# Kernel tuning notes

Hardware: AMD Instinct MI355X
Metric: run time of the kernel (lower is better)

Reference implementation:

```python
import jax, jax.numpy as jnp
import numpy as np

EPS = 1e-6  # torch.nn.CosineSimilarity eps


def _emb_sum(table, ids):
    # ids: (N, L) int -> (N, D): gather rows then sum over tokens (EmbeddingBag-sum)
    return table[ids].sum(axis=1)


def _cos_rows(q, M):
    # cosine similarity of vector q (D,) against each row of M (N, D), torch eps semantics:
    # dot / max(||a||*||b||, eps)
    num = M @ q
    den = jnp.maximum(jnp.linalg.norm(M, axis=1) * jnp.linalg.norm(q), EPS)
    return num / den


def setup_inputs() -> dict:
    key = jax.random.key(0)
    ks = jax.random.split(key, 10)
    V, D = 50000, 128
    N_MEM, N_CAND, N_PERS, L, LQ = 65536, 10000, 20, 20, 32
    return {
        "xs": jax.random.randint(ks[0], (1, LQ), 0, V, dtype=jnp.int32),
        "candidates": jax.random.randint(ks[1], (N_CAND, L), 0, V, dtype=jnp.int32),
        "persona": jax.random.randint(ks[2], (N_PERS, L), 0, V, dtype=jnp.int32),
        "keys": jax.random.randint(ks[3], (N_MEM, L), 0, V, dtype=jnp.int32),
        "values": jax.random.randint(ks[4], (N_MEM, L), 0, V, dtype=jnp.int32),
        "label": jax.random.randint(ks[5], (1, LQ), 0, V, dtype=jnp.int32),
        "shared_emb": jax.random.normal(ks[6], (V, D), dtype=jnp.float32),
        "cand_emb": jax.random.normal(ks[7], (V, D), dtype=jnp.float32),
        "R_W": jax.random.normal(ks[8], (D, D), dtype=jnp.float32) * (1.0 / np.sqrt(D)),
        "R2_W": jax.random.normal(ks[9], (D, D), dtype=jnp.float32) * (1.0 / np.sqrt(D)),
    }


def reference(xs, candidates, persona, keys, values, label, shared_emb, cand_emb, R_W, R2_W):
    enc_keys = _emb_sum(shared_emb, keys)        # (N_mem, D)
    enc_values = _emb_sum(shared_emb, values)    # (N_mem, D)
    enc_cands = _emb_sum(cand_emb, candidates)   # (N_cand, D)
    enc_pers = _emb_sum(shared_emb, persona)     # (N_pers, D)

    q = shared_emb[xs].sum(axis=1).reshape(-1)   # (D,)

    for W in (R_W, R2_W):  # loop is hardcoded to 2 hops in the source
        att = jax.nn.softmax(_cos_rows(q, enc_pers))          # (N_pers,)
        hop = (att[:, None] * enc_pers).sum(axis=0)           # (D,)
        q_plus = (q + hop) @ W.T                               # Linear no bias
        att = jax.nn.softmax(_cos_rows(q_plus, enc_keys))     # (N_mem,)
        hop = (att[:, None] * enc_values).sum(axis=0)         # (D,)
        q = (q_plus + hop) @ W.T

    preds = _cos_rows(q, enc_cands)  # (N_cand,)
    return preds
```

## Files before the change

### kernel.cpp

```cpp
#include <hip/hip_runtime.h>
#include <math.h>
#include <stdint.h>

#define D 128
#define EPS 1e-6f
typedef unsigned short u16;


__device__ __forceinline__ float wave_sum(float v) {
#pragma unroll
    for (int off = 32; off > 0; off >>= 1) v += __shfl_xor(v, off, 64);
    return v;
}
__device__ __forceinline__ float halfwave_sum(float v) {
#pragma unroll
    for (int off = 16; off > 0; off >>= 1) v += __shfl_xor(v, off, 32);
    return v;
}

__device__ __forceinline__ float bf2f(u16 h) {
    union { unsigned u; float f; } x;
    x.u = ((unsigned)h) << 16;
    return x.f;
}
__device__ __forceinline__ float bflo(unsigned u) { return bf2f((u16)(u & 0xffff)); }
__device__ __forceinline__ float bfhi(unsigned u) { return bf2f((u16)(u >> 16)); }
__device__ __forceinline__ u16 f2bf(float f) {
    union { float f; unsigned u; } x;
    x.f = f;
    unsigned u = x.u;
    return (u16)((u + 0x7fff + ((u >> 16) & 1)) >> 16);
}
__device__ __forceinline__ unsigned pack2(float a, float b) {
    return (unsigned)f2bf(a) | ((unsigned)f2bf(b) << 16);
}

__global__ void prep_k(const float* __restrict__ semb, u16* __restrict__ tbl,
                       int V, const int* __restrict__ pers, int NP,
                       const int* __restrict__ xs, int LQ,
                       float* __restrict__ enc_pers, float* __restrict__ pnorms,
                       float* __restrict__ st, int nbA) {
    const int tid = threadIdx.x;
    const int bid = blockIdx.x;
    if (bid < nbA) {
        const int n = V * 64;
        const int stride = nbA * 256;
        for (int i = bid * 256 + tid; i < n; i += stride) {
            const int v = i >> 6;
            const int c2 = i & 63;
            const float2 ab = *(const float2*)(semb + (long)v * D + 2 * c2);
            *(unsigned*)(tbl + (long)v * D + 2 * c2) = pack2(ab.x, ab.y);
        }
    } else {
        const int lane = tid & 63;
        const int half = lane >> 5;
        const int hl = lane & 31;
        const int w0 = (bid - nbA) * 4 + (tid >> 6);
        const int npr = NP + 1;
        const int npairs = (npr + 1) >> 1;
        for (int w = w0; w < npairs; w += 12) {
            const int row = 2 * w + half;
            const bool valid = row < npr;
            const int rowc = valid ? row : NP;
            const bool isq = (rowc == NP);
            const int* ids = isq ? xs : (pers + (long)rowc * 20);
            const int L = isq ? LQ : 20;
            int myid = 0;
            if (hl < L) myid = ids[hl];
            float4 acc = {0.f, 0.f, 0.f, 0.f};
            for (int t = 0; t < L; ++t) {
                const int idx = __shfl(myid, (half << 5) + t, 64);
                const float4 e = *(const float4*)(semb + (long)idx * D + 4 * hl);
                acc.x += e.x; acc.y += e.y; acc.z += e.z; acc.w += e.w;
            }
            if (valid) {
                float* outp = isq ? st : (enc_pers + (long)rowc * D);
                *(float4*)(outp + 4 * hl) = acc;
                float sq = acc.x * acc.x + acc.y * acc.y + acc.z * acc.z + acc.w * acc.w;
                sq = halfwave_sum(sq);
                if (hl == 0) {
                    if (isq) st[384] = sqrtf(sq);
                    else pnorms[rowc] = sqrtf(sq);
                }
            }
        }
    }
}

__device__ void persona_dev(const float* __restrict__ pers_rows,
                            const float* __restrict__ pnorms,
                            const float* __restrict__ W, float* __restrict__ st,
                            int NP, float* smem, int tid) {
    float* qsh = smem;
    float* qh = smem + 128;
    float* att = smem + 256;
    float* red = smem + 320;
    if (tid < D) qsh[tid] = st[tid];
    __syncthreads();
    if (tid < NP) {
        float dot = 0.f;
        const float* pr = pers_rows + (long)tid * D;
        for (int d2 = 0; d2 < D; ++d2) dot += pr[d2] * qsh[d2];
        att[tid] = dot / fmaxf(pnorms[tid] * st[384], EPS);
    }
    __syncthreads();
    if (tid == 0) {
        float m = -1e30f;
        for (int p = 0; p < NP; ++p) m = fmaxf(m, att[p]);
        float s = 0.f;
        for (int p = 0; p < NP; ++p) { att[p] = __expf(att[p] - m); s += att[p]; }
        float inv = 1.f / s;
        for (int p = 0; p < NP; ++p) att[p] *= inv;
    }
    __syncthreads();
    if (tid < D) {
        float h = 0.f;
        for (int p = 0; p < NP; ++p) h += att[p] * pers_rows[(long)p * D + tid];
        qh[tid] = qsh[tid] + h;
    }
    __syncthreads();
    float qp = 0.f;
    if (tid < D) {
        for (int d2 = 0; d2 < D; ++d2) qp += W[(long)tid * D + d2] * qh[d2];
        st[128 + tid] = qp;
    }
    float sq = wave_sum(qp * qp);
    if ((tid & 63) == 0 && tid < 128) red[tid >> 6] = sq;
    __syncthreads();
    if (tid == 0) st[385] = sqrtf(red[0] + red[1]);
    if (tid < D) st[256 + tid] = 0.f;
    if (tid < D) st[512 + tid] = 0.f;
    if (tid == 0) { st[386] = 0.f; st[640] = 0.f; }
}

__device__ void mid_dev_s(const float* __restrict__ W1, const float* __restrict__ W2,
                          const float* __restrict__ pers_rows,
                          const float* __restrict__ pnorms,
                          const float* __restrict__ st,
                          float* __restrict__ qp_out, float* __restrict__ qpn_out,
                          float* smem, int tid, int NP) {
    float* qh = smem;
    float* qsh = smem + 128;
    float* att = smem + 256;
    float* red = smem + 320;
    const float inv = 1.f / st[386];
    if (tid < D) qh[tid] = st[128 + tid] + st[256 + tid] * inv;
    __syncthreads();
    float qn = 0.f;
    if (tid < D) {
        for (int d2 = 0; d2 < D; ++d2) qn += W1[(long)tid * D + d2] * qh[d2];
        qsh[tid] = qn;
    }
    float sq = wave_sum(qn * qn);
    if ((tid & 63) == 0 && tid < 128) red[tid >> 6] = sq;
    __syncthreads();
    const float qnorm = sqrtf(red[0] + red[1]);
    if (tid < NP) {
        float dot = 0.f;
        for (int d2 = 0; d2 < D; ++d2) dot += pers_rows[(long)tid * D + d2] * qsh[d2];
        att[tid] = dot / fmaxf(pnorms[tid] * qnorm, EPS);
    }
    __syncthreads();
    if (tid == 0) {
        float m = -1e30f;
        for (int p = 0; p < NP; ++p) m = fmaxf(m, att[p]);
        float s = 0.f;
        for (int p = 0; p < NP; ++p) { att[p] = __expf(att[p] - m); s += att[p]; }
        float is = 1.f / s;
        for (int p = 0; p < NP; ++p) att[p] *= is;
    }
    __syncthreads();
    if (tid < D) {
        float h = 0.f;
        for (int p = 0; p < NP; ++p) h += att[p] * pers_rows[(long)p * D + tid];
        qh[tid] = qsh[tid] + h;
    }
    __syncthreads();
    float qp = 0.f;
    if (tid < D) {
        for (int d2 = 0; d2 < D; ++d2) qp += W2[(long)tid * D + d2] * qh[d2];
        qp_out[tid] = qp;
    }
    float sq2 = wave_sum(qp * qp);
    if ((tid & 63) == 0 && tid < 128) red[tid >> 6] = sq2;
    __syncthreads();
    if (tid == 0) *qpn_out = sqrtf(red[0] + red[1]);
    __syncthreads();
}

__global__ void kvp_k(const u16* __restrict__ tbl, const int* __restrict__ kids,
                      const int* __restrict__ vids, int N,
                      float* __restrict__ kb, u16* __restrict__ vb,
                      float* __restrict__ knorms,
                      const float* __restrict__ enc_pers,
                      const float* __restrict__ pnorms,
                      const float* __restrict__ RW, float* __restrict__ st,
                      int NP) {
    __shared__ float smem[336];
    const int tid = threadIdx.x;
    const int bid = blockIdx.x;
    if (bid == 0) {
        persona_dev(enc_pers, pnorms, RW, st, NP, smem, tid);
        return;
    }
    const int lane = tid & 63;
    const int half = lane >> 5;
    const int hl = lane & 31;
    const int ghw = ((bid - 1) * 256 + tid) >> 5;
    const int nhw = ((gridDim.x - 1) * 256) >> 5;
    for (int i = ghw; i < N; i += nhw) {
        int kid = 0, vid = 0;
        if (hl < 20) {
            kid = kids[(long)i * 20 + hl];
            vid = vids[(long)i * 20 + hl];
        }
        float k0 = 0.f, k1 = 0.f, k2 = 0.f, k3 = 0.f;
        float v0 = 0.f, v1 = 0.f, v2 = 0.f, v3 = 0.f;
#pragma unroll
        for (int t = 0; t < 20; ++t) {
            const int kj = __shfl(kid, (half << 5) + t, 64);
            const int vj = __shfl(vid, (half << 5) + t, 64);
            const ushort4 ke = *(const ushort4*)(tbl + (long)kj * D + 4 * hl);
            const ushort4 ve = *(const ushort4*)(tbl + (long)vj * D + 4 * hl);
            k0 += bf2f(ke.x); k1 += bf2f(ke.y); k2 += bf2f(ke.z); k3 += bf2f(ke.w);
            v0 += bf2f(ve.x); v1 += bf2f(ve.y); v2 += bf2f(ve.z); v3 += bf2f(ve.w);
        }
        float4 kr;
        kr.x = k0; kr.y = k1; kr.z = k2; kr.w = k3;
        *(float4*)(kb + (long)i * D + 4 * hl) = kr;
        uint2 pv;
        pv.x = pack2(v0, v1);
        pv.y = pack2(v2, v3);
        *(uint2*)(vb + (long)i * D + 4 * hl) = pv;
        float sq = halfwave_sum(k0 * k0 + k1 * k1 + k2 * k2 + k3 * k3);
        if (hl == 0) knorms[i] = sqrtf(sq);
    }
}

__global__ void attcv2_k(const float* __restrict__ kb, const u16* __restrict__ vb,
                         const float* __restrict__ knorms,
                         const float* __restrict__ W1, const float* __restrict__ W2,
                         const float* __restrict__ enc_pers,
                         const float* __restrict__ pnorms,
                         float* __restrict__ st, int N, int NP, int hop) {
    __shared__ float msm[324];
    __shared__ float qp_s[128];
    __shared__ float qpn_s;
    __shared__ float rsm[129];
    const int tid = threadIdx.x;
    if (hop == 0) {
        if (tid < 128) qp_s[tid] = st[128 + tid];
        if (tid == 0) qpn_s = st[385];
    } else {
        mid_dev_s(W1, W2, enc_pers, pnorms, st, qp_s, &qpn_s, msm, tid, NP);
    }
    __syncthreads();
    const int lane = tid & 63;
    const int half = lane >> 5;
    const int hl = lane & 31;
    const float4 qp4 = *(const float4*)(qp_s + 4 * hl);
    const float qpn = qpn_s;
    const int aoff = hop ? 512 : 256;
    const int eoff = hop ? 640 : 386;
    const int ghw = (int)((blockIdx.x * blockDim.x + tid) >> 5);
    const int nhw = (int)((gridDim.x * blockDim.x) >> 5);
    float a0 = 0.f, a1 = 0.f, a2 = 0.f, a3 = 0.f;
    float esum = 0.f;
    for (int i = ghw; i < N; i += nhw) {
        const float4 kr = *(const float4*)(kb + (long)i * D + 4 * hl);
        const float part = kr.x * qp4.x + kr.y * qp4.y + kr.z * qp4.z + kr.w * qp4.w;
        const float dot = halfwave_sum(part);
        const float c = dot / fmaxf(knorms[i] * qpn, EPS);
        const float e = __expf(c);
        const uint2 vh = *(const uint2*)(vb + (long)i * D + 4 * hl);
        a0 += e * bflo(vh.x);
        a1 += e * bfhi(vh.x);
        a2 += e * bflo(vh.y);
        a3 += e * bfhi(vh.y);
        if (hl == 0) esum += e;
    }
    a0 += __shfl_xor(a0, 32, 64);
    a1 += __shfl_xor(a1, 32, 64);
    a2 += __shfl_xor(a2, 32, 64);
    a3 += __shfl_xor(a3, 32, 64);
    esum += __shfl_xor(esum, 32, 64);
    if (tid < 129) rsm[tid] = 0.f;
    __syncthreads();
    if (half == 0) {
        atomicAdd(&rsm[4 * hl + 0], a0);
        atomicAdd(&rsm[4 * hl + 1], a1);
        atomicAdd(&rsm[4 * hl + 2], a2);
        atomicAdd(&rsm[4 * hl + 3], a3);
        if (hl == 0) atomicAdd(&rsm[128], esum);
    }
    __syncthreads();
    if (tid < 128) atomicAdd(&st[aoff + tid], rsm[tid]);
    if (tid == 128) atomicAdd(&st[eoff], rsm[128]);
}

__global__ void k5f(const float* __restrict__ W1, const float* __restrict__ W2,
                    const float* __restrict__ enc_pers,
                    const float* __restrict__ pnorms,
                    const float* __restrict__ cemb,
                    const int* __restrict__ cands, int NC, int NP,
                    const float* __restrict__ st, float* __restrict__ out) {
    __shared__ float msm[324];
    __shared__ float qp2_s[128];
    __shared__ float qpn2_s;
    __shared__ float qhf[128];
    __shared__ float qv[D];
    __shared__ float red2[2];
    __shared__ float qns;
    const int tid = threadIdx.x;
    mid_dev_s(W1, W2, enc_pers, pnorms, st, qp2_s, &qpn2_s, msm, tid, NP);
    const float inv2 = 1.f / st[640];
    if (tid < D) qhf[tid] = qp2_s[tid] + st[512 + tid] * inv2;
    __syncthreads();
    float qn = 0.f;
    if (tid < D) {
        for (int d2 = 0; d2 < D; ++d2) qn += W2[(long)tid * D + d2] * qhf[d2];
        qv[tid] = qn;
    }
    float sq = wave_sum(qn * qn);
    if ((tid & 63) == 0 && tid < 128) red2[tid >> 6] = sq;
    __syncthreads();
    if (tid == 0) qns = sqrtf(red2[0] + red2[1]);
    __syncthreads();
    const int lane = tid & 63;
    const int half = lane >> 5;
    const int hl = lane & 31;
    const int gw = (int)((blockIdx.x * blockDim.x + tid) >> 6);
    const int nw = (int)((gridDim.x * blockDim.x) >> 6);
    const float4 q4 = *(const float4*)(qv + 4 * hl);
    const float qnf = qns;
    const int npair = (NC + 1) >> 1;
    for (int p = gw; p < npair; p += nw) {
        const int row = 2 * p + half;
        const bool valid = row < NC;
        const int rowc = valid ? row : (NC - 1);
        int myid = 0;
        if (hl < 20) myid = cands[(long)rowc * 20 + hl];
        float4 acc = {0.f, 0.f, 0.f, 0.f};
#pragma unroll
        for (int t = 0; t < 20; ++t) {
            const int idx = __shfl(myid, (half << 5) + t, 64);
            const float4 e = *(const float4*)(cemb + (long)idx * D + 4 * hl);
            acc.x += e.x; acc.y += e.y; acc.z += e.z; acc.w += e.w;
        }
        float dot = halfwave_sum(acc.x * q4.x + acc.y * q4.y +
                                 acc.z * q4.z + acc.w * q4.w);
        float nsq = halfwave_sum(acc.x * acc.x + acc.y * acc.y +
                                 acc.z * acc.z + acc.w * acc.w);
        if (valid && hl == 0) out[row] = dot / fmaxf(sqrtf(nsq) * qnf, EPS);
    }
}

__global__ void encode_small_p(const float* __restrict__ emb,
                               const int* __restrict__ pers, int NP, int LP,
                               const int* __restrict__ xs, int LQ,
                               float* __restrict__ pers_rows,
                               float* __restrict__ pnorms,
                               float* __restrict__ st) {
    const int lane = threadIdx.x & 63;
    const int half = lane >> 5;
    const int hl = lane & 31;
    int gw = (int)((blockIdx.x * blockDim.x + threadIdx.x) >> 6);
    int nw = (int)((gridDim.x * blockDim.x) >> 6);
    const int npr = NP + 1;
    const int npairs = (npr + 1) >> 1;
    for (int p = gw; p < npairs; p += nw) {
        const int row = 2 * p + half;
        const bool valid = row < npr;
        const int rowc = valid ? row : NP;
        const bool isq = (rowc == NP);
        const int* ids = isq ? xs : (pers + (long)rowc * LP);
        const int L = isq ? LQ : LP;
        int myid = 0;
        if (hl < L) myid = ids[hl];
        float4 acc = {0.f, 0.f, 0.f, 0.f};
        for (int t = 0; t < L; ++t) {
            const int idx = __shfl(myid, (half << 5) + t, 64);
            const float4 e = *(const float4*)(emb + (long)idx * D + 4 * hl);
            acc.x += e.x; acc.y += e.y; acc.z += e.z; acc.w += e.w;
        }
        if (valid) {
            float* outp = isq ? st : (pers_rows + (long)rowc * D);
            *(float4*)(outp + 4 * hl) = acc;
            float sq = acc.x * acc.x + acc.y * acc.y + acc.z * acc.z + acc.w * acc.w;
            sq = halfwave_sum(sq);
            if (hl == 0) {
                if (isq) st[384] = sqrtf(sq);
                else pnorms[rowc] = sqrtf(sq);
            }
        }
    }
}

__global__ void persona_hop(const float* __restrict__ pers_rows,
                            const float* __restrict__ pnorms,
                            const float* __restrict__ W,
                            float* __restrict__ st, int NP) {
    __shared__ float smem[336];
    persona_dev(pers_rows, pnorms, W, st, NP, smem, (int)threadIdx.x);
}

__global__ void mid_hop(const float* __restrict__ W1, const float* __restrict__ W2,
                        const float* __restrict__ pers_rows,
                        const float* __restrict__ pnorms,
                        float* __restrict__ st, int NP) {
    __shared__ float qh[D];
    __shared__ float qsh[D];
    __shared__ float att[64];
    __shared__ float red[2];
    int tid = threadIdx.x;
    float inv = 1.f / st[386];
    qh[tid] = st[128 + tid] + st[256 + tid] * inv;
    __syncthreads();
    float qn = 0.f;
    for (int d2 = 0; d2 < D; ++d2) qn += W1[tid * D + d2] * qh[d2];
    qsh[tid] = qn;
    st[tid] = qn;
    float sq = wave_sum(qn * qn);
    if ((tid & 63) == 0) red[tid >> 6] = sq;
    __syncthreads();
    float qnorm = sqrtf(red[0] + red[1]);
    if (tid == 0) st[384] = qnorm;
    if (tid < NP) {
        float dot = 0.f;
        for (int d2 = 0; d2 < D; ++d2) dot += pers_rows[tid * D + d2] * qsh[d2];
        att[tid] = dot / fmaxf(pnorms[tid] * qnorm, EPS);
    }
    __syncthreads();
    if (tid == 0) {
        float m = -1e30f;
        for (int p = 0; p < NP; ++p) m = fmaxf(m, att[p]);
        float s = 0.f;
        for (int p = 0; p < NP; ++p) { att[p] = __expf(att[p] - m); s += att[p]; }
        float is = 1.f / s;
        for (int p = 0; p < NP; ++p) att[p] *= is;
    }
    __syncthreads();
    float h = 0.f;
    for (int p = 0; p < NP; ++p) h += att[p] * pers_rows[p * D + tid];
    qh[tid] = qsh[tid] + h;
    __syncthreads();
    float qp = 0.f;
    for (int d2 = 0; d2 < D; ++d2) qp += W2[tid * D + d2] * qh[d2];
    st[128 + tid] = qp;
    float sq2 = wave_sum(qp * qp);
    if ((tid & 63) == 0) red[tid >> 6] = sq2;
    __syncthreads();
    if (tid == 0) st[385] = sqrtf(red[0] + red[1]);
    st[256 + tid] = 0.f;
    if (tid == 0) st[386] = 0.f;
}

__global__ void finish_hop(const float* __restrict__ W, float* __restrict__ st) {
    __shared__ float qh[D];
    __shared__ float red[2];
    int tid = threadIdx.x;
    float inv = 1.f / st[386];
    qh[tid] = st[128 + tid] + st[256 + tid] * inv;
    __syncthreads();
    float qn = 0.f;
    for (int d2 = 0; d2 < D; ++d2) qn += W[tid * D + d2] * qh[d2];
    st[tid] = qn;
    float sq = wave_sum(qn * qn);
    if ((tid & 63) == 0) red[tid >> 6] = sq;
    __syncthreads();
    if (tid == 0) st[384] = sqrtf(red[0] + red[1]);
}

__global__ void k5_final(const float* __restrict__ cemb,
                         const int* __restrict__ cands, int NC,
                         const float* __restrict__ st, float* __restrict__ out) {
    const int lane = threadIdx.x & 63;
    const int half = lane >> 5;
    const int hl = lane & 31;
    const int gw = (int)((blockIdx.x * blockDim.x + threadIdx.x) >> 6);
    const int nw = (int)((gridDim.x * blockDim.x) >> 6);
    const float4 q4 = *(const float4*)(st + 4 * hl);
    const float qn = st[384];
    const int npair = (NC + 1) >> 1;
    for (int p = gw; p < npair; p += nw) {
        const int row = 2 * p + half;
        const bool valid = row < NC;
        const int rowc = valid ? row : (NC - 1);
        int myid = 0;
        if (hl < 20) myid = cands[(long)rowc * 20 + hl];
        float4 acc = {0.f, 0.f, 0.f, 0.f};
#pragma unroll
        for (int t = 0; t < 20; ++t) {
            const int idx = __shfl(myid, (half << 5) + t, 64);
            const float4 e = *(const float4*)(cemb + (long)idx * D + 4 * hl);
            acc.x += e.x; acc.y += e.y; acc.z += e.z; acc.w += e.w;
        }
        float dot = halfwave_sum(acc.x * q4.x + acc.y * q4.y +
                                 acc.z * q4.z + acc.w * q4.w);
        float nsq = halfwave_sum(acc.x * acc.x + acc.y * acc.y +
                                 acc.z * acc.z + acc.w * acc.w);
        if (valid && hl == 0) out[row] = dot / fmaxf(sqrtf(nsq) * qn, EPS);
    }
}

__global__ void big_att_rc(const float* __restrict__ emb,
                           const int* __restrict__ kids,
                           const int* __restrict__ vids,
                           float* __restrict__ st, int N) {
    __shared__ float s[129];
    const int tid = threadIdx.x;
    const int lane = tid & 63;
    const int half = lane >> 5;
    const int hl = lane & 31;
    const int gw = (int)((blockIdx.x * blockDim.x + tid) >> 6);
    const int nw = (int)((gridDim.x * blockDim.x) >> 6);
    const float4 qp = *(const float4*)(st + 128 + 4 * hl);
    const float qpn = st[385];
    float4 hacc = {0.f, 0.f, 0.f, 0.f};
    float esum = 0.f;
    const int npair = (N + 1) >> 1;
    for (int p = gw; p < npair; p += nw) {
        const int row = 2 * p + half;
        const bool valid = row < N;
        const int rowc = valid ? row : (N - 1);
        int kid = 0, vid = 0;
        if (hl < 20) {
            kid = kids[(long)rowc * 20 + hl];
            vid = vids[(long)rowc * 20 + hl];
        }
        float4 ka = {0.f, 0.f, 0.f, 0.f}, va = {0.f, 0.f, 0.f, 0.f};
#pragma unroll
        for (int t = 0; t < 20; ++t) {
            const int ki = __shfl(kid, (half << 5) + t, 64);
            const int vi = __shfl(vid, (half << 5) + t, 64);
            const float4 ke = *(const float4*)(emb + (long)ki * D + 4 * hl);
            const float4 ve = *(const float4*)(emb + (long)vi * D + 4 * hl);
            ka.x += ke.x; ka.y += ke.y; ka.z += ke.z; ka.w += ke.w;
            va.x += ve.x; va.y += ve.y; va.z += ve.z; va.w += ve.w;
        }
        float nsq = halfwave_sum(ka.x * ka.x + ka.y * ka.y + ka.z * ka.z + ka.w * ka.w);
        float dot = halfwave_sum(ka.x * qp.x + ka.y * qp.y + ka.z * qp.z + ka.w * qp.w);
        const float c = dot / fmaxf(sqrtf(nsq) * qpn, EPS);
        float e = __expf(c);
        if (!valid) e = 0.f;
        hacc.x += e * va.x; hacc.y += e * va.y;
        hacc.z += e * va.z; hacc.w += e * va.w;
        if (hl == 0) esum += e;
    }
    hacc.x += __shfl_xor(hacc.x, 32, 64);
    hacc.y += __shfl_xor(hacc.y, 32, 64);
    hacc.z += __shfl_xor(hacc.z, 32, 64);
    hacc.w += __shfl_xor(hacc.w, 32, 64);
    esum += __shfl_xor(esum, 32, 64);
    if (tid < 129) s[tid] = 0.f;
    __syncthreads();
    if (half == 0) {
        atomicAdd(&s[4 * hl + 0], hacc.x);
        atomicAdd(&s[4 * hl + 1], hacc.y);
        atomicAdd(&s[4 * hl + 2], hacc.z);
        atomicAdd(&s[4 * hl + 3], hacc.w);
        if (hl == 0) atomicAdd(&s[128], esum);
    }
    __syncthreads();
    if (tid < 128) atomicAdd(&st[256 + tid], s[tid]);
    if (tid == 128) atomicAdd(&st[386], s[128]);
}

static inline size_t align16(size_t b) { return (b + 15) & ~(size_t)15; }

extern "C" void kernel_launch(void* const* d_in, const int* in_sizes, int n_in,
                              void* d_out, int out_size, void* d_ws, size_t ws_size,
                              hipStream_t stream) {
    const int* xs = (const int*)d_in[0];
    const int* cands = (const int*)d_in[1];
    const int* pers = (const int*)d_in[2];
    const int* keys = (const int*)d_in[3];
    const int* values = (const int*)d_in[4];
    const float* semb = (const float*)d_in[6];
    const float* cemb = (const float*)d_in[7];
    const float* RW = (const float*)d_in[8];
    const float* R2W = (const float*)d_in[9];
    float* out = (float*)d_out;

    const int L = 20;
    const int LQ = in_sizes[0];
    const int VD = in_sizes[6];
    const int V = VD / D;
    const int NMEM = in_sizes[3] / L;
    const int NCAND = in_sizes[1] / L;
    const int NPERS = in_sizes[2] / L;

    size_t need = align16((size_t)VD * 2) + align16((size_t)NMEM * D * 2) +
                  align16((size_t)NMEM * D * 4) + align16((size_t)NMEM * 4) +
                  align16((size_t)NPERS * D * 4) + align16((size_t)NPERS * 4) +
                  1024 * 4;
    bool stored = (d_ws != nullptr) && (ws_size >= need) && (NMEM % 4 == 0) &&
                  (NMEM <= 65536) && ((VD & 3) == 0) && (LQ <= 32) &&
                  (NPERS <= 64);

    const int THR = 256;
    char* base = (char*)d_ws;
    u16 *tbl16 = nullptr, *vb = nullptr;
    float *kb = nullptr, *knorms = nullptr;
    if (stored) {
        tbl16 = (u16*)base;  base += align16((size_t)VD * 2);
        vb = (u16*)base;     base += align16((size_t)NMEM * D * 2);
        kb = (float*)base;   base += align16((size_t)NMEM * D * 4);
        knorms = (float*)base; base += align16((size_t)NMEM * 4);
    }
    float* enc_pers = (float*)base; base += align16((size_t)NPERS * D * 4);
    float* pnorms = (float*)base;   base += align16((size_t)NPERS * 4);
    float* st = (float*)base;

    if (stored) {
        const int nbA = 2048;
        prep_k<<<nbA + 3, THR, 0, stream>>>(semb, tbl16, V, pers, NPERS, xs, LQ,
                                            enc_pers, pnorms, st, nbA);
        kvp_k<<<2048, THR, 0, stream>>>(tbl16, keys, values, NMEM, kb, vb,
                                        knorms, enc_pers, pnorms, RW, st, NPERS);
        attcv2_k<<<1024, THR, 0, stream>>>(kb, vb, knorms, RW, R2W, enc_pers,
                                           pnorms, st, NMEM, NPERS, 0);
        attcv2_k<<<1024, THR, 0, stream>>>(kb, vb, knorms, RW, R2W, enc_pers,
                                           pnorms, st, NMEM, NPERS, 1);
        k5f<<<640, THR, 0, stream>>>(RW, R2W, enc_pers, pnorms, cemb, cands,
                                     NCAND, NPERS, st, out);
        (void)n_in; (void)out_size;
        return;
    }

    {
        int npairs = (NPERS + 2) / 2;
        int blocks = (npairs + 3) / 4;
        encode_small_p<<<blocks, THR, 0, stream>>>(semb, pers, NPERS, L, xs,
                                                   LQ, enc_pers, pnorms, st);
    }
    persona_hop<<<1, 128, 0, stream>>>(enc_pers, pnorms, RW, st, NPERS);
    big_att_rc<<<1024, THR, 0, stream>>>(semb, keys, values, st, NMEM);
    mid_hop<<<1, 128, 0, stream>>>(RW, R2W, enc_pers, pnorms, st, NPERS);
    big_att_rc<<<1024, THR, 0, stream>>>(semb, keys, values, st, NMEM);
    finish_hop<<<1, 128, 0, stream>>>(R2W, st);
    int nblk5 = (((NCAND + 1) / 2) + 3) / 4;
    k5_final<<<nblk5, THR, 0, stream>>>(cemb, cands, NCAND, st, out);

    (void)n_in; (void)out_size;
}
```

Measured before the change: 321.6 us.

## Spread attention atomics over 16 buckets and split key/value encoding kernels

```diff
diff --git a/kernel.cpp b/kernel.cpp
--- a/kernel.cpp
+++ b/kernel.cpp
@@ -5,6 +5,11 @@
 #define D 128
 #define EPS 1e-6f
 typedef unsigned short u16;
+
+#define NBK 16
+#define BSTR 132
+#define H1OFF 512
+#define H2OFF (512 + NBK * BSTR)
 
 
 __device__ __forceinline__ float wave_sum(float v) {
@@ -90,7 +95,7 @@
 __device__ void persona_dev(const float* __restrict__ pers_rows,
                             const float* __restrict__ pnorms,
                             const float* __restrict__ W, float* __restrict__ st,
-                            int NP, float* smem, int tid) {
+                            int NP, float* smem, int tid, int zb) {
     float* qsh = smem;
     float* qh = smem + 128;
     float* att = smem + 256;
@@ -128,9 +133,13 @@
     if ((tid & 63) == 0 && tid < 128) red[tid >> 6] = sq;
     __syncthreads();
     if (tid == 0) st[385] = sqrtf(red[0] + red[1]);
-    if (tid < D) st[256 + tid] = 0.f;
-    if (tid < D) st[512 + tid] = 0.f;
-    if (tid == 0) { st[386] = 0.f; st[640] = 0.f; }
+    if (zb) {
+        for (int i = tid; i < 2 * NBK * BSTR; i += (int)blockDim.x)
+            st[H1OFF + i] = 0.f;
+    } else {
+        if (tid < D) st[256 + tid] = 0.f;
+        if (tid == 0) st[386] = 0.f;
+    }
 }
 
 __device__ void mid_dev_s(const float* __restrict__ W1, const float* __restrict__ W2,
@@ -143,8 +152,16 @@
     float* qsh = smem + 128;
     float* att = smem + 256;
     float* red = smem + 320;
-    const float inv = 1.f / st[386];
-    if (tid < D) qh[tid] = st[128 + tid] + st[256 + tid] * inv;
+    float esum = 0.f;
+#pragma unroll
+    for (int b = 0; b < NBK; ++b) esum += st[H1OFF + b * BSTR + 128];
+    const float inv = 1.f / esum;
+    if (tid < D) {
+        float a = 0.f;
+#pragma unroll
+        for (int b = 0; b < NBK; ++b) a += st[H1OFF + b * BSTR + tid];
+        qh[tid] = st[128 + tid] + a * inv;
+    }
     __syncthreads();
     float qn = 0.f;
     if (tid < D) {
@@ -188,19 +205,17 @@
     __syncthreads();
 }
 
-__global__ void kvp_k(const u16* __restrict__ tbl, const int* __restrict__ kids,
-                      const int* __restrict__ vids, int N,
-                      float* __restrict__ kb, u16* __restrict__ vb,
-                      float* __restrict__ knorms,
-                      const float* __restrict__ enc_pers,
-                      const float* __restrict__ pnorms,
-                      const float* __restrict__ RW, float* __restrict__ st,
-                      int NP) {
+__global__ void kv_k(const u16* __restrict__ tbl, const int* __restrict__ kids,
+                     int N, float* __restrict__ kb, float* __restrict__ knorms,
+                     const float* __restrict__ enc_pers,
+                     const float* __restrict__ pnorms,
+                     const float* __restrict__ RW, float* __restrict__ st,
+                     int NP) {
     __shared__ float smem[336];
     const int tid = threadIdx.x;
     const int bid = blockIdx.x;
     if (bid == 0) {
-        persona_dev(enc_pers, pnorms, RW, st, NP, smem, tid);
+        persona_dev(enc_pers, pnorms, RW, st, NP, smem, tid, 1);
         return;
     }
     const int lane = tid & 63;
@@ -209,31 +224,46 @@
     const int ghw = ((bid - 1) * 256 + tid) >> 5;
     const int nhw = ((gridDim.x - 1) * 256) >> 5;
     for (int i = ghw; i < N; i += nhw) {
-        int kid = 0, vid = 0;
-        if (hl < 20) {
-            kid = kids[(long)i * 20 + hl];
-            vid = vids[(long)i * 20 + hl];
-        }
+        int kid = 0;
+        if (hl < 20) kid = kids[(long)i * 20 + hl];
         float k0 = 0.f, k1 = 0.f, k2 = 0.f, k3 = 0.f;
-        float v0 = 0.f, v1 = 0.f, v2 = 0.f, v3 = 0.f;
 #pragma unroll
         for (int t = 0; t < 20; ++t) {
             const int kj = __shfl(kid, (half << 5) + t, 64);
-            const int vj = __shfl(vid, (half << 5) + t, 64);
             const ushort4 ke = *(const ushort4*)(tbl + (long)kj * D + 4 * hl);
-            const ushort4 ve = *(const ushort4*)(tbl + (long)vj * D + 4 * hl);
             k0 += bf2f(ke.x); k1 += bf2f(ke.y); k2 += bf2f(ke.z); k3 += bf2f(ke.w);
-            v0 += bf2f(ve.x); v1 += bf2f(ve.y); v2 += bf2f(ve.z); v3 += bf2f(ve.w);
         }
         float4 kr;
         kr.x = k0; kr.y = k1; kr.z = k2; kr.w = k3;
         *(float4*)(kb + (long)i * D + 4 * hl) = kr;
+        float sq = halfwave_sum(k0 * k0 + k1 * k1 + k2 * k2 + k3 * k3);
+        if (hl == 0) knorms[i] = sqrtf(sq);
+    }
+}
+
+__global__ void kv_v(const u16* __restrict__ tbl, const int* __restrict__ vids,
+                     int N, u16* __restrict__ vb) {
+    const int tid = threadIdx.x;
+    const int bid = blockIdx.x;
+    const int lane = tid & 63;
+    const int half = lane >> 5;
+    const int hl = lane & 31;
+    const int ghw = (bid * 256 + tid) >> 5;
+    const int nhw = (gridDim.x * 256) >> 5;
+    for (int i = ghw; i < N; i += nhw) {
+        int vid = 0;
+        if (hl < 20) vid = vids[(long)i * 20 + hl];
+        float v0 = 0.f, v1 = 0.f, v2 = 0.f, v3 = 0.f;
+#pragma unroll
+        for (int t = 0; t < 20; ++t) {
+            const int vj = __shfl(vid, (half << 5) + t, 64);
+            const ushort4 ve = *(const ushort4*)(tbl + (long)vj * D + 4 * hl);
+            v0 += bf2f(ve.x); v1 += bf2f(ve.y); v2 += bf2f(ve.z); v3 += bf2f(ve.w);
+        }
         uint2 pv;
         pv.x = pack2(v0, v1);
         pv.y = pack2(v2, v3);
         *(uint2*)(vb + (long)i * D + 4 * hl) = pv;
-        float sq = halfwave_sum(k0 * k0 + k1 * k1 + k2 * k2 + k3 * k3);
-        if (hl == 0) knorms[i] = sqrtf(sq);
     }
 }
 
@@ -260,8 +290,7 @@
     const int hl = lane & 31;
     const float4 qp4 = *(const float4*)(qp_s + 4 * hl);
     const float qpn = qpn_s;
-    const int aoff = hop ? 512 : 256;
-    const int eoff = hop ? 640 : 386;
+    const int aoff = (hop ? H2OFF : H1OFF) + (int)(blockIdx.x & (NBK - 1)) * BSTR;
     const int ghw = (int)((blockIdx.x * blockDim.x + tid) >> 5);
     const int nhw = (int)((gridDim.x * blockDim.x) >> 5);
     float a0 = 0.f, a1 = 0.f, a2 = 0.f, a3 = 0.f;
@@ -295,7 +324,7 @@
     }
     __syncthreads();
     if (tid < 128) atomicAdd(&st[aoff + tid], rsm[tid]);
-    if (tid == 128) atomicAdd(&st[eoff], rsm[128]);
+    if (tid == 128) atomicAdd(&st[aoff + 128], rsm[128]);
 }
 
 __global__ void k5f(const float* __restrict__ W1, const float* __restrict__ W2,
@@ -313,8 +342,16 @@
     __shared__ float qns;
     const int tid = threadIdx.x;
     mid_dev_s(W1, W2, enc_pers, pnorms, st, qp2_s, &qpn2_s, msm, tid, NP);
-    const float inv2 = 1.f / st[640];
-    if (tid < D) qhf[tid] = qp2_s[tid] + st[512 + tid] * inv2;
+    float esum2 = 0.f;
+#pragma unroll
+    for (int b = 0; b < NBK; ++b) esum2 += st[H2OFF + b * BSTR + 128];
+    const float inv2 = 1.f / esum2;
+    if (tid < D) {
+        float a = 0.f;
+#pragma unroll
+        for (int b = 0; b < NBK; ++b) a += st[H2OFF + b * BSTR + tid];
+        qhf[tid] = qp2_s[tid] + a * inv2;
+    }
     __syncthreads();
     float qn = 0.f;
     if (tid < D) {
@@ -401,7 +438,7 @@
                             const float* __restrict__ W,
                             float* __restrict__ st, int NP) {
     __shared__ float smem[336];
-    persona_dev(pers_rows, pnorms, W, st, NP, smem, (int)threadIdx.x);
+    persona_dev(pers_rows, pnorms, W, st, NP, smem, (int)threadIdx.x, 0);
 }
 
 __global__ void mid_hop(const float* __restrict__ W1, const float* __restrict__ W2,
@@ -593,7 +630,7 @@
     size_t need = align16((size_t)VD * 2) + align16((size_t)NMEM * D * 2) +
                   align16((size_t)NMEM * D * 4) + align16((size_t)NMEM * 4) +
                   align16((size_t)NPERS * D * 4) + align16((size_t)NPERS * 4) +
-                  1024 * 4;
+                  8192 * 4;
     bool stored = (d_ws != nullptr) && (ws_size >= need) && (NMEM % 4 == 0) &&
                   (NMEM <= 65536) && ((VD & 3) == 0) && (LQ <= 32) &&
                   (NPERS <= 64);
@@ -616,8 +653,9 @@
         const int nbA = 2048;
         prep_k<<<nbA + 3, THR, 0, stream>>>(semb, tbl16, V, pers, NPERS, xs, LQ,
                                             enc_pers, pnorms, st, nbA);
-        kvp_k<<<2048, THR, 0, stream>>>(tbl16, keys, values, NMEM, kb, vb,
-                                        knorms, enc_pers, pnorms, RW, st, NPERS);
+        kv_k<<<2049, THR, 0, stream>>>(tbl16, keys, NMEM, kb, knorms,
+                                       enc_pers, pnorms, RW, st, NPERS);
+        kv_v<<<2048, THR, 0, stream>>>(tbl16, values, NMEM, vb);
         attcv2_k<<<1024, THR, 0, stream>>>(kb, vb, knorms, RW, R2W, enc_pers,
                                            pnorms, st, NMEM, NPERS, 0);
         attcv2_k<<<1024, THR, 0, stream>>>(kb, vb, knorms, RW, R2W, enc_pers,
```

Result: faster. 269.1 us (-16.3%).
